# Kernel optimization log

Measured on AMD Instinct MI355X. Metric: run time of the kernel, lower is better.

## Reference

```python
import jax, jax.numpy as jnp
import numpy as np

B, N, D, H = 32, 64, 128, 256

def setup_inputs() -> dict:
    key = jax.random.key(0)
    ks = jax.random.split(key, 6)
    s = 0.02
    return {
        "objects": jax.random.normal(ks[0], (B, N, D), dtype=jnp.float32),
        "gW1": jax.random.normal(ks[1], (2 * D, H), dtype=jnp.float32) * s,
        "gb1": jnp.zeros((H,), dtype=jnp.float32),
        "gW2": jax.random.normal(ks[2], (H, H), dtype=jnp.float32) * s,
        "gb2": jnp.zeros((H,), dtype=jnp.float32),
        "gW3": jax.random.normal(ks[3], (H, H), dtype=jnp.float32) * s,
        "gb3": jnp.zeros((H,), dtype=jnp.float32),
        "fW1": jax.random.normal(ks[4], (H, H), dtype=jnp.float32) * s,
        "fb1": jnp.zeros((H,), dtype=jnp.float32),
        "fW2": jax.random.normal(ks[5], (H, H), dtype=jnp.float32) * s,
        "fb2": jnp.zeros((H,), dtype=jnp.float32),
    }

def reference(objects, gW1, gb1, gW2, gb2, gW3, gb3, fW1, fb1, fW2, fb2):
    b, n, d = objects.shape
    # Pairwise concat: pair[b,i,j] = [objects[b,i], objects[b,j]] -> (B,N,N,2D)
    left = jnp.broadcast_to(objects[:, :, None, :], (b, n, n, d))
    right = jnp.broadcast_to(objects[:, None, :, :], (b, n, n, d))
    pair = jnp.concatenate([left, right], axis=-1)
    # g_theta: 3-layer MLP with ReLU after first two layers
    h = jax.nn.relu(pair @ gW1 + gb1)
    h = jax.nn.relu(h @ gW2 + gb2)
    h = h @ gW3 + gb3                      # (B,N,N,H)
    # Sum over all pairs i != j
    mask = (1.0 - jnp.eye(n, dtype=h.dtype))  # (N,N)
    agg = jnp.einsum('bijh,ij->bh', h, mask)  # (B,H)
    # f_phi: Linear-ReLU-Linear
    out = jax.nn.relu(agg @ fW1 + fb1) @ fW2 + fb2
    return out
```

## Files before the change

### kernel.cpp

```cpp
#include <hip/hip_runtime.h>
#include <hip/hip_bf16.h>

typedef __attribute__((ext_vector_type(8))) _Float16 half8;
typedef __attribute__((ext_vector_type(4))) float f32x4;

__global__ __launch_bounds__(256) void rn_prep(
    const float* __restrict__ obj, const float* __restrict__ gW1,
    const float* __restrict__ gb1, const float* __restrict__ gW2,
    const float* __restrict__ gW3, const float* __restrict__ gb3,
    const float* __restrict__ fW1, const float* __restrict__ fb1,
    _Float16* __restrict__ Lh, char* __restrict__ RhB,
    _Float16* __restrict__ W2h, float* __restrict__ S,
    float* __restrict__ M, float* __restrict__ dvec)
{
    __shared__ float so[8 * 128];
    __shared__ float tt[64 * 65];
    __shared__ float sg[8][256];
    const int blk = blockIdx.x, t = threadIdx.x;

    if (blk < 256) {
        const int r0 = blk * 8;
        #pragma unroll
        for (int it = 0; it < 4; ++it) so[it * 256 + t] = obj[r0 * 128 + it * 256 + t];
        __syncthreads();
        float accL[8], accR[8];
        #pragma unroll
        for (int r = 0; r < 8; ++r) { accL[r] = 0.f; accR[r] = 0.f; }
        for (int k = 0; k < 128; ++k) {
            float wL = gW1[k * 256 + t];
            float wR = gW1[(128 + k) * 256 + t];
            #pragma unroll
            for (int r = 0; r < 8; ++r) {
                float o = so[r * 128 + k];
                accL[r] += o * wL;
                accR[r] += o * wR;
            }
        }
        float bb = gb1[t];
        #pragma unroll
        for (int r = 0; r < 8; ++r) {
            int row = r0 + r;
            Lh[row * 256 + t] = (_Float16)(accL[r] + bb);
            *(_Float16*)(RhB + row * 512 + ((2 * t) ^ ((row & 15) << 4))) = (_Float16)accR[r];
        }
    } else if (blk < 272) {
        const int tb = blk - 256;
        const int k0 = (tb >> 2) * 64, c0 = (tb & 3) * 64;
        for (int it = 0; it < 16; ++it) {
            int idx = it * 256 + t, rr = idx >> 6, cc = idx & 63;
            tt[rr * 65 + cc] = gW2[(k0 + rr) * 256 + c0 + cc];
        }
        __syncthreads();
        for (int it = 0; it < 16; ++it) {
            int idx = it * 256 + t, cr = idx >> 6, kk = idx & 63;
            W2h[(c0 + cr) * 256 + (k0 + kk)] = (_Float16)tt[kk * 65 + cr];
        }
    } else if (blk == 272) {
        for (int it = 0; it < 32; ++it) S[it * 256 + t] = 0.f;
        float a = 0.f;
        for (int j = 0; j < 256; ++j) a += gb3[j] * fW1[j * 256 + t];
        dvec[t] = 4032.0f * a + fb1[t];
    } else {
        const int r0 = (blk - 273) * 8;
        #pragma unroll
        for (int it = 0; it < 8; ++it) sg[it][t] = gW3[(r0 + it) * 256 + t];
        __syncthreads();
        float acc[8];
        #pragma unroll
        for (int r = 0; r < 8; ++r) acc[r] = 0.f;
        for (int j = 0; j < 256; ++j) {
            float wv = fW1[j * 256 + t];
            #pragma unroll
            for (int r = 0; r < 8; ++r) acc[r] += sg[r][j] * wv;
        }
        #pragma unroll
        for (int r = 0; r < 8; ++r) M[(r0 + r) * 256 + t] = acc[r];
    }
}

__global__ __launch_bounds__(512, 2) void rn_main(
    const char* __restrict__ LhB, const char* __restrict__ RhB,
    const _Float16* __restrict__ W2h, const float* __restrict__ gb2,
    float* __restrict__ S)
{
    __shared__ __attribute__((aligned(16))) char smem[36864];
    const int blk = blockIdx.x;
    const int b = blk >> 3, ig = blk & 7;
    const int t = threadIdx.x, lane = t & 63, w = t >> 6;
    const int mg = w >> 2, ng = w & 3;
    const int lc = lane & 15, lg = lane >> 4;

    {
        const char* gR = RhB + b * 32768;
        #pragma unroll
        for (int it = 0; it < 4; ++it) {
            int u = it * 512 + t;
            *(f32x4*)(smem + u * 16) = *(const f32x4*)(gR + u * 16);
        }
        if (t < 256) {
            const char* gL = LhB + (b * 64 + ig * 8) * 512;
            *(f32x4*)(smem + 32768 + t * 16) = *(const f32x4*)(gL + t * 16);
        }
    }

    half8 bfr[4][8];
    #pragma unroll
    for (int n = 0; n < 4; ++n)
        #pragma unroll
        for (int ks = 0; ks < 8; ++ks)
            bfr[n][ks] = *(const half8*)(W2h + (ng * 64 + n * 16 + lc) * 256 + ks * 32 + lg * 8);

    float bias[4];
    #pragma unroll
    for (int n = 0; n < 4; ++n) bias[n] = gb2[ng * 64 + n * 16 + lc];

    __syncthreads();

    half8 rh[2][8];
    #pragma unroll
    for (int m2 = 0; m2 < 2; ++m2) {
        int row = mg * 32 + m2 * 16 + lc;
        #pragma unroll
        for (int ks = 0; ks < 8; ++ks) {
            int kb = ks * 64 + lg * 16;
            rh[m2][ks] = *(const half8*)(smem + row * 512 + (kb ^ (lc << 4)));
        }
    }

    const half8 zero8 = {(_Float16)0.f, (_Float16)0.f, (_Float16)0.f, (_Float16)0.f,
                         (_Float16)0.f, (_Float16)0.f, (_Float16)0.f, (_Float16)0.f};
    float csum[4] = {0.f, 0.f, 0.f, 0.f};

    for (int ii = 0; ii < 8; ++ii) {
        f32x4 acc[2][4];
        #pragma unroll
        for (int m2 = 0; m2 < 2; ++m2)
            #pragma unroll
            for (int n = 0; n < 4; ++n)
                acc[m2][n] = (f32x4){0.f, 0.f, 0.f, 0.f};

        #pragma unroll
        for (int ks = 0; ks < 8; ++ks) {
            half8 lhv = *(const half8*)(smem + 32768 + ii * 512 + ks * 64 + lg * 16);
            #pragma unroll
            for (int m2 = 0; m2 < 2; ++m2) {
                half8 av = lhv + rh[m2][ks];
                av = __builtin_elementwise_max(av, zero8);
                #pragma unroll
                for (int n = 0; n < 4; ++n)
                    acc[m2][n] = __builtin_amdgcn_mfma_f32_16x16x32_f16(
                        av, bfr[n][ks], acc[m2][n], 0, 0, 0);
            }
        }

        const int iglob = ig * 8 + ii;
        #pragma unroll
        for (int n = 0; n < 4; ++n) {
            float cs = 0.f;
            #pragma unroll
            for (int m2 = 0; m2 < 2; ++m2)
                #pragma unroll
                for (int q = 0; q < 4; ++q) {
                    int row = mg * 32 + m2 * 16 + lg * 4 + q;
                    float v = fmaxf(acc[m2][n][q] + bias[n], 0.f);
                    cs += (row == iglob) ? 0.f : v;
                }
            csum[n] += cs;
        }
    }

    #pragma unroll
    for (int n = 0; n < 4; ++n) {
        float cs = csum[n];
        cs += __shfl_xor(cs, 16);
        cs += __shfl_xor(cs, 32);
        if (lane < 16) atomicAdd(&S[b * 256 + ng * 64 + n * 16 + lc], cs);
    }
}

__global__ __launch_bounds__(1024) void rn_final(
    const float* __restrict__ S, const float* __restrict__ M,
    const float* __restrict__ dvec, const float* __restrict__ fW2,
    const float* __restrict__ fb2, float* __restrict__ out)
{
    __shared__ float vec[256];
    __shared__ float ps[16][260];
    const int b = blockIdx.x, t = threadIdx.x;
    const int cg = t & 63, kq = t >> 6;
    const int c0 = cg * 4;

    if (t < 256) vec[t] = S[b * 256 + t];
    __syncthreads();

    f32x4 w2r[16];
    {
        f32x4 s = (f32x4){0.f, 0.f, 0.f, 0.f};
        #pragma unroll
        for (int kk = 0; kk < 16; ++kk) {
            int k = kq * 16 + kk;
            s += (*(const f32x4*)&M[k * 256 + c0]) * vec[k];
        }
        *(f32x4*)&ps[kq][c0] = s;
        #pragma unroll
        for (int kk = 0; kk < 16; ++kk)
            w2r[kk] = *(const f32x4*)&fW2[(kq * 16 + kk) * 256 + c0];
    }
    __syncthreads();
    if (t < 256) {
        float a = 0.f;
        #pragma unroll
        for (int q = 0; q < 16; ++q) a += ps[q][t];
        vec[t] = fmaxf(a + dvec[t], 0.f);
    }
    __syncthreads();

    {
        f32x4 s = (f32x4){0.f, 0.f, 0.f, 0.f};
        #pragma unroll
        for (int kk = 0; kk < 16; ++kk)
            s += w2r[kk] * vec[kq * 16 + kk];
        *(f32x4*)&ps[kq][c0] = s;
    }
    __syncthreads();
    if (t < 256) {
        float a = 0.f;
        #pragma unroll
        for (int q = 0; q < 16; ++q) a += ps[q][t];
        out[b * 256 + t] = a + fb2[t];
    }
}

extern "C" void kernel_launch(void* const* d_in, const int* in_sizes, int n_in,
                              void* d_out, int out_size, void* d_ws, size_t ws_size,
                              hipStream_t stream)
{
    const float* obj = (const float*)d_in[0];
    const float* gW1 = (const float*)d_in[1];
    const float* gb1 = (const float*)d_in[2];
    const float* gW2 = (const float*)d_in[3];
    const float* gb2 = (const float*)d_in[4];
    const float* gW3 = (const float*)d_in[5];
    const float* gb3 = (const float*)d_in[6];
    const float* fW1 = (const float*)d_in[7];
    const float* fb1 = (const float*)d_in[8];
    const float* fW2 = (const float*)d_in[9];
    const float* fb2 = (const float*)d_in[10];
    float* out = (float*)d_out;

    char* ws = (char*)d_ws;
    _Float16* Lh  = (_Float16*)(ws);
    char*     RhB = ws + (1u << 20);
    _Float16* W2h = (_Float16*)(ws + (2u << 20));
    float*    S   = (float*)(ws + (2u << 20) + (128u << 10));
    float*    M   = (float*)(ws + (2u << 20) + (160u << 10));
    float*    dv  = (float*)(ws + (2u << 20) + (416u << 10));

    rn_prep <<<305, 256, 0, stream>>>(obj, gW1, gb1, gW2, gW3, gb3, fW1, fb1,
                                      Lh, RhB, W2h, S, M, dv);
    rn_main <<<256, 512, 0, stream>>>((const char*)Lh, RhB, W2h, gb2, S);
    rn_final<<<32, 1024, 0, stream>>>(S, M, dv, fW2, fb2, out);
}
```

Before: 47.95 us.

## Drop LDS staging in main kernel and vectorize prep GEMV blocks with split-K

```diff
diff --git a/kernel.cpp b/kernel.cpp
--- a/kernel.cpp
+++ b/kernel.cpp
@@ -9,13 +9,14 @@
     const float* __restrict__ gb1, const float* __restrict__ gW2,
     const float* __restrict__ gW3, const float* __restrict__ gb3,
     const float* __restrict__ fW1, const float* __restrict__ fb1,
-    _Float16* __restrict__ Lh, char* __restrict__ RhB,
+    _Float16* __restrict__ Lh, _Float16* __restrict__ Rh,
     _Float16* __restrict__ W2h, float* __restrict__ S,
     float* __restrict__ M, float* __restrict__ dvec)
 {
     __shared__ float so[8 * 128];
     __shared__ float tt[64 * 65];
-    __shared__ float sg[8][256];
+    __shared__ float sg[8 * 256];
+    __shared__ float ps[4][8][256];
     const int blk = blockIdx.x, t = threadIdx.x;
 
     if (blk < 256) {
@@ -41,7 +42,7 @@
         for (int r = 0; r < 8; ++r) {
             int row = r0 + r;
             Lh[row * 256 + t] = (_Float16)(accL[r] + bb);
-            *(_Float16*)(RhB + row * 512 + ((2 * t) ^ ((row & 15) << 4))) = (_Float16)accR[r];
+            Rh[row * 256 + t] = (_Float16)accR[r];
         }
     } else if (blk < 272) {
         const int tb = blk - 256;
@@ -57,52 +58,53 @@
         }
     } else if (blk == 272) {
         for (int it = 0; it < 32; ++it) S[it * 256 + t] = 0.f;
-        float a = 0.f;
-        for (int j = 0; j < 256; ++j) a += gb3[j] * fW1[j * 256 + t];
-        dvec[t] = 4032.0f * a + fb1[t];
+        const int cg = t & 63, jq = t >> 6, c0 = cg * 4;
+        f32x4 a = (f32x4){0.f, 0.f, 0.f, 0.f};
+        #pragma unroll 8
+        for (int jj = 0; jj < 64; ++jj) {
+            int j = jq * 64 + jj;
+            a += gb3[j] * (*(const f32x4*)&fW1[j * 256 + c0]);
+        }
+        *(f32x4*)&ps[jq][0][c0] = a;
+        __syncthreads();
+        float s = ps[0][0][t] + ps[1][0][t] + ps[2][0][t] + ps[3][0][t];
+        dvec[t] = 4032.0f * s + fb1[t];
     } else {
         const int r0 = (blk - 273) * 8;
-        #pragma unroll
-        for (int it = 0; it < 8; ++it) sg[it][t] = gW3[(r0 + it) * 256 + t];
-        __syncthreads();
-        float acc[8];
-        #pragma unroll
-        for (int r = 0; r < 8; ++r) acc[r] = 0.f;
-        for (int j = 0; j < 256; ++j) {
-            float wv = fW1[j * 256 + t];
-            #pragma unroll
-            for (int r = 0; r < 8; ++r) acc[r] += sg[r][j] * wv;
-        }
-        #pragma unroll
-        for (int r = 0; r < 8; ++r) M[(r0 + r) * 256 + t] = acc[r];
+        const int cg = t & 63, jq = t >> 6, c0 = cg * 4;
+        #pragma unroll
+        for (int it = 0; it < 8; ++it) sg[it * 256 + t] = gW3[(r0 + it) * 256 + t];
+        __syncthreads();
+        f32x4 acc[8];
+        #pragma unroll
+        for (int r = 0; r < 8; ++r) acc[r] = (f32x4){0.f, 0.f, 0.f, 0.f};
+        #pragma unroll 8
+        for (int jj = 0; jj < 64; ++jj) {
+            int j = jq * 64 + jj;
+            f32x4 wv = *(const f32x4*)&fW1[j * 256 + c0];
+            #pragma unroll
+            for (int r = 0; r < 8; ++r) acc[r] += sg[r * 256 + j] * wv;
+        }
+        #pragma unroll
+        for (int r = 0; r < 8; ++r) *(f32x4*)&ps[jq][r][c0] = acc[r];
+        __syncthreads();
+        #pragma unroll
+        for (int r = 0; r < 8; ++r)
+            M[(r0 + r) * 256 + t] = ps[0][r][t] + ps[1][r][t] + ps[2][r][t] + ps[3][r][t];
     }
 }
 
 __global__ __launch_bounds__(512, 2) void rn_main(
-    const char* __restrict__ LhB, const char* __restrict__ RhB,
+    const _Float16* __restrict__ Lh, const _Float16* __restrict__ Rh,
     const _Float16* __restrict__ W2h, const float* __restrict__ gb2,
     float* __restrict__ S)
 {
-    __shared__ __attribute__((aligned(16))) char smem[36864];
     const int blk = blockIdx.x;
     const int b = blk >> 3, ig = blk & 7;
     const int t = threadIdx.x, lane = t & 63, w = t >> 6;
     const int mg = w >> 2, ng = w & 3;
     const int lc = lane & 15, lg = lane >> 4;
 
-    {
-        const char* gR = RhB + b * 32768;
-        #pragma unroll
-        for (int it = 0; it < 4; ++it) {
-            int u = it * 512 + t;
-            *(f32x4*)(smem + u * 16) = *(const f32x4*)(gR + u * 16);
-        }
-        if (t < 256) {
-            const char* gL = LhB + (b * 64 + ig * 8) * 512;
-            *(f32x4*)(smem + 32768 + t * 16) = *(const f32x4*)(gL + t * 16);
-        }
-    }
-
     half8 bfr[4][8];
     #pragma unroll
     for (int n = 0; n < 4; ++n)
@@ -110,42 +112,41 @@
         for (int ks = 0; ks < 8; ++ks)
             bfr[n][ks] = *(const half8*)(W2h + (ng * 64 + n * 16 + lc) * 256 + ks * 32 + lg * 8);
 
+    half8 rh[2][8];
+    #pragma unroll
+    for (int m2 = 0; m2 < 2; ++m2) {
+        int row = b * 64 + mg * 32 + m2 * 16 + lc;
+        #pragma unroll
+        for (int ks = 0; ks < 8; ++ks)
+            rh[m2][ks] = *(const half8*)(Rh + row * 256 + ks * 32 + lg * 8);
+    }
+
     float bias[4];
     #pragma unroll
     for (int n = 0; n < 4; ++n) bias[n] = gb2[ng * 64 + n * 16 + lc];
 
-    __syncthreads();
-
-    half8 rh[2][8];
-    #pragma unroll
-    for (int m2 = 0; m2 < 2; ++m2) {
-        int row = mg * 32 + m2 * 16 + lc;
-        #pragma unroll
-        for (int ks = 0; ks < 8; ++ks) {
-            int kb = ks * 64 + lg * 16;
-            rh[m2][ks] = *(const half8*)(smem + row * 512 + (kb ^ (lc << 4)));
-        }
-    }
-
+    const _Float16* lbase = Lh + (b * 64 + ig * 8) * 256;
     const half8 zero8 = {(_Float16)0.f, (_Float16)0.f, (_Float16)0.f, (_Float16)0.f,
                          (_Float16)0.f, (_Float16)0.f, (_Float16)0.f, (_Float16)0.f};
+    const f32x4 zero4 = (f32x4){0.f, 0.f, 0.f, 0.f};
     float csum[4] = {0.f, 0.f, 0.f, 0.f};
-
+    const int rgbase = mg * 32 + lg * 4;
+
+    #pragma unroll
     for (int ii = 0; ii < 8; ++ii) {
         f32x4 acc[2][4];
         #pragma unroll
         for (int m2 = 0; m2 < 2; ++m2)
             #pragma unroll
             for (int n = 0; n < 4; ++n)
-                acc[m2][n] = (f32x4){0.f, 0.f, 0.f, 0.f};
+                acc[m2][n] = zero4;
 
         #pragma unroll
         for (int ks = 0; ks < 8; ++ks) {
-            half8 lhv = *(const half8*)(smem + 32768 + ii * 512 + ks * 64 + lg * 16);
+            half8 lhv = *(const half8*)(lbase + ii * 256 + ks * 32 + lg * 8);
             #pragma unroll
             for (int m2 = 0; m2 < 2; ++m2) {
-                half8 av = lhv + rh[m2][ks];
-                av = __builtin_elementwise_max(av, zero8);
+                half8 av = __builtin_elementwise_max(lhv + rh[m2][ks], zero8);
                 #pragma unroll
                 for (int n = 0; n < 4; ++n)
                     acc[m2][n] = __builtin_amdgcn_mfma_f32_16x16x32_f16(
@@ -156,16 +157,15 @@
         const int iglob = ig * 8 + ii;
         #pragma unroll
         for (int n = 0; n < 4; ++n) {
-            float cs = 0.f;
-            #pragma unroll
-            for (int m2 = 0; m2 < 2; ++m2)
-                #pragma unroll
-                for (int q = 0; q < 4; ++q) {
-                    int row = mg * 32 + m2 * 16 + lg * 4 + q;
-                    float v = fmaxf(acc[m2][n][q] + bias[n], 0.f);
-                    cs += (row == iglob) ? 0.f : v;
-                }
-            csum[n] += cs;
+            f32x4 bv = (f32x4){bias[n], bias[n], bias[n], bias[n]};
+            #pragma unroll
+            for (int m2 = 0; m2 < 2; ++m2) {
+                f32x4 v = __builtin_elementwise_max(acc[m2][n] + bv, zero4);
+                float cs = (v[0] + v[1]) + (v[2] + v[3]);
+                if (rgbase + m2 * 16 == (iglob & ~3))
+                    cs -= v[ii & 3];
+                csum[n] += cs;
+            }
         }
     }
 
@@ -249,14 +249,14 @@
 
     char* ws = (char*)d_ws;
     _Float16* Lh  = (_Float16*)(ws);
-    char*     RhB = ws + (1u << 20);
+    _Float16* Rh  = (_Float16*)(ws + (1u << 20));
     _Float16* W2h = (_Float16*)(ws + (2u << 20));
     float*    S   = (float*)(ws + (2u << 20) + (128u << 10));
     float*    M   = (float*)(ws + (2u << 20) + (160u << 10));
     float*    dv  = (float*)(ws + (2u << 20) + (416u << 10));
 
     rn_prep <<<305, 256, 0, stream>>>(obj, gW1, gb1, gW2, gW3, gb3, fW1, fb1,
-                                      Lh, RhB, W2h, S, M, dv);
-    rn_main <<<256, 512, 0, stream>>>((const char*)Lh, RhB, W2h, gb2, S);
+                                      Lh, Rh, W2h, S, M, dv);
+    rn_main <<<256, 512, 0, stream>>>(Lh, Rh, W2h, gb2, S);
     rn_final<<<32, 1024, 0, stream>>>(S, M, dv, fW2, fb2, out);
 }
```

Result: slower. 142.5 us (+197.1%).

## Split final MLP into two wide kernels and separate prep block roles

Applied to the files above, without the earlier changes.

```diff
diff --git a/kernel.cpp b/kernel.cpp
--- a/kernel.cpp
+++ b/kernel.cpp
@@ -3,6 +3,11 @@
 
 typedef __attribute__((ext_vector_type(8))) _Float16 half8;
 typedef __attribute__((ext_vector_type(4))) float f32x4;
+
+union PrepShared {
+    struct { float so[8 * 128]; float tt[64 * 65]; } a;
+    struct { float sg[8 * 256]; } m;
+};
 
 __global__ __launch_bounds__(256) void rn_prep(
     const float* __restrict__ obj, const float* __restrict__ gW1,
@@ -13,12 +18,11 @@
     _Float16* __restrict__ W2h, float* __restrict__ S,
     float* __restrict__ M, float* __restrict__ dvec)
 {
-    __shared__ float so[8 * 128];
-    __shared__ float tt[64 * 65];
-    __shared__ float sg[8][256];
+    __shared__ PrepShared sh;
     const int blk = blockIdx.x, t = threadIdx.x;
 
     if (blk < 256) {
+        float* so = sh.a.so;
         const int r0 = blk * 8;
         #pragma unroll
         for (int it = 0; it < 4; ++it) so[it * 256 + t] = obj[r0 * 128 + it * 256 + t];
@@ -44,6 +48,7 @@
             *(_Float16*)(RhB + row * 512 + ((2 * t) ^ ((row & 15) << 4))) = (_Float16)accR[r];
         }
     } else if (blk < 272) {
+        float* tt = sh.a.tt;
         const int tb = blk - 256;
         const int k0 = (tb >> 2) * 64, c0 = (tb & 3) * 64;
         for (int it = 0; it < 16; ++it) {
@@ -56,22 +61,27 @@
             W2h[(c0 + cr) * 256 + (k0 + kk)] = (_Float16)tt[kk * 65 + cr];
         }
     } else if (blk == 272) {
+        #pragma unroll
         for (int it = 0; it < 32; ++it) S[it * 256 + t] = 0.f;
+    } else if (blk == 273) {
         float a = 0.f;
+        #pragma unroll 8
         for (int j = 0; j < 256; ++j) a += gb3[j] * fW1[j * 256 + t];
         dvec[t] = 4032.0f * a + fb1[t];
     } else {
-        const int r0 = (blk - 273) * 8;
-        #pragma unroll
-        for (int it = 0; it < 8; ++it) sg[it][t] = gW3[(r0 + it) * 256 + t];
+        float* sg = sh.m.sg;
+        const int r0 = (blk - 274) * 8;
+        #pragma unroll
+        for (int it = 0; it < 8; ++it) sg[it * 256 + t] = gW3[(r0 + it) * 256 + t];
         __syncthreads();
         float acc[8];
         #pragma unroll
         for (int r = 0; r < 8; ++r) acc[r] = 0.f;
+        #pragma unroll 4
         for (int j = 0; j < 256; ++j) {
             float wv = fW1[j * 256 + t];
             #pragma unroll
-            for (int r = 0; r < 8; ++r) acc[r] += sg[r][j] * wv;
+            for (int r = 0; r < 8; ++r) acc[r] += sg[r * 256 + j] * wv;
         }
         #pragma unroll
         for (int r = 0; r < 8; ++r) M[(r0 + r) * 256 + t] = acc[r];
@@ -144,8 +154,7 @@
             half8 lhv = *(const half8*)(smem + 32768 + ii * 512 + ks * 64 + lg * 16);
             #pragma unroll
             for (int m2 = 0; m2 < 2; ++m2) {
-                half8 av = lhv + rh[m2][ks];
-                av = __builtin_elementwise_max(av, zero8);
+                half8 av = __builtin_elementwise_max(lhv + rh[m2][ks], zero8);
                 #pragma unroll
                 for (int n = 0; n < 4; ++n)
                     acc[m2][n] = __builtin_amdgcn_mfma_f32_16x16x32_f16(
@@ -178,55 +187,61 @@
     }
 }
 
-__global__ __launch_bounds__(1024) void rn_final(
+__global__ __launch_bounds__(256) void rn_final1(
     const float* __restrict__ S, const float* __restrict__ M,
-    const float* __restrict__ dvec, const float* __restrict__ fW2,
+    const float* __restrict__ dvec, float* __restrict__ u)
+{
+    __shared__ float vec[256];
+    __shared__ float ps[8][36];
+    const int b = blockIdx.x >> 3, cg = blockIdx.x & 7;
+    const int t = threadIdx.x;
+    const int cl = t & 31, kq = t >> 5;
+    const int c = cg * 32 + cl;
+
+    vec[t] = S[b * 256 + t];
+    __syncthreads();
+    float s = 0.f;
+    #pragma unroll
+    for (int kk = 0; kk < 32; ++kk) {
+        int k = kq * 32 + kk;
+        s += vec[k] * M[k * 256 + c];
+    }
+    ps[kq][cl] = s;
+    __syncthreads();
+    if (t < 32) {
+        float a = 0.f;
+        #pragma unroll
+        for (int q = 0; q < 8; ++q) a += ps[q][t];
+        u[b * 256 + cg * 32 + t] = fmaxf(a + dvec[cg * 32 + t], 0.f);
+    }
+}
+
+__global__ __launch_bounds__(256) void rn_final2(
+    const float* __restrict__ u, const float* __restrict__ fW2,
     const float* __restrict__ fb2, float* __restrict__ out)
 {
     __shared__ float vec[256];
-    __shared__ float ps[16][260];
-    const int b = blockIdx.x, t = threadIdx.x;
-    const int cg = t & 63, kq = t >> 6;
-    const int c0 = cg * 4;
-
-    if (t < 256) vec[t] = S[b * 256 + t];
-    __syncthreads();
-
-    f32x4 w2r[16];
-    {
-        f32x4 s = (f32x4){0.f, 0.f, 0.f, 0.f};
-        #pragma unroll
-        for (int kk = 0; kk < 16; ++kk) {
-            int k = kq * 16 + kk;
-            s += (*(const f32x4*)&M[k * 256 + c0]) * vec[k];
-        }
-        *(f32x4*)&ps[kq][c0] = s;
-        #pragma unroll
-        for (int kk = 0; kk < 16; ++kk)
-            w2r[kk] = *(const f32x4*)&fW2[(kq * 16 + kk) * 256 + c0];
-    }
-    __syncthreads();
-    if (t < 256) {
+    __shared__ float ps[8][36];
+    const int b = blockIdx.x >> 3, cg = blockIdx.x & 7;
+    const int t = threadIdx.x;
+    const int cl = t & 31, kq = t >> 5;
+    const int c = cg * 32 + cl;
+
+    vec[t] = u[b * 256 + t];
+    __syncthreads();
+    float s = 0.f;
+    #pragma unroll
+    for (int kk = 0; kk < 32; ++kk) {
+        int k = kq * 32 + kk;
+        s += vec[k] * fW2[k * 256 + c];
+    }
+    ps[kq][cl] = s;
+    __syncthreads();
+    if (t < 32) {
         float a = 0.f;
         #pragma unroll
-        for (int q = 0; q < 16; ++q) a += ps[q][t];
-        vec[t] = fmaxf(a + dvec[t], 0.f);
-    }
-    __syncthreads();
-
-    {
-        f32x4 s = (f32x4){0.f, 0.f, 0.f, 0.f};
-        #pragma unroll
-        for (int kk = 0; kk < 16; ++kk)
-            s += w2r[kk] * vec[kq * 16 + kk];
-        *(f32x4*)&ps[kq][c0] = s;
-    }
-    __syncthreads();
-    if (t < 256) {
-        float a = 0.f;
-        #pragma unroll
-        for (int q = 0; q < 16; ++q) a += ps[q][t];
-        out[b * 256 + t] = a + fb2[t];
+        for (int q = 0; q < 8; ++q) a += ps[q][t];
+        out[b * 256 + cg * 32 + t] = a + fb2[cg * 32 + t];
     }
 }
 
@@ -254,9 +269,11 @@
     float*    S   = (float*)(ws + (2u << 20) + (128u << 10));
     float*    M   = (float*)(ws + (2u << 20) + (160u << 10));
     float*    dv  = (float*)(ws + (2u << 20) + (416u << 10));
-
-    rn_prep <<<305, 256, 0, stream>>>(obj, gW1, gb1, gW2, gW3, gb3, fW1, fb1,
-                                      Lh, RhB, W2h, S, M, dv);
-    rn_main <<<256, 512, 0, stream>>>((const char*)Lh, RhB, W2h, gb2, S);
-    rn_final<<<32, 1024, 0, stream>>>(S, M, dv, fW2, fb2, out);
-}
+    float*    uB  = (float*)(ws + (2u << 20) + (420u << 10));
+
+    rn_prep  <<<306, 256, 0, stream>>>(obj, gW1, gb1, gW2, gW3, gb3, fW1, fb1,
+                                       Lh, RhB, W2h, S, M, dv);
+    rn_main  <<<256, 512, 0, stream>>>((const char*)Lh, RhB, W2h, gb2, S);
+    rn_final1<<<256, 256, 0, stream>>>(S, M, dv, uB);
+    rn_final2<<<256, 256, 0, stream>>>(uB, fW2, fb2, out);
+}
```

Result: slower. 50.61 us (+5.6%).
